# Performance work log

Measured on AMD Instinct MI355X. Metric: run time of the kernel, lower is better.

The kernel has to match this reference:

```python
import jax, jax.numpy as jnp
import numpy as np

N_NODES = 50000
N_EDGES = 800000
IN_DIM = 64
HEADS = 8
OUT_DIM = 8
CLAMP = 5.0
EPS = 1e-8


def _xavier(key, shape, fan_in, fan_out):
    std = float(np.sqrt(2.0 / (fan_in + fan_out)))
    return jax.random.normal(key, shape, jnp.float32) * std


def setup_inputs() -> dict:
    key = jax.random.key(0)
    ks = jax.random.split(key, 16)
    HD = HEADS * OUT_DIM
    return {
        "x": jax.random.normal(ks[0], (N_NODES, IN_DIM), jnp.float32),
        "edge_attr": jax.random.normal(ks[1], (N_EDGES, IN_DIM), jnp.float32),
        "edge_index": jax.random.randint(ks[2], (2, N_EDGES), 0, N_NODES, jnp.int64),
        "Wq": _xavier(ks[3], (IN_DIM, HD), IN_DIM, HD),
        "bq": jnp.zeros((HD,), jnp.float32),
        "Wk": _xavier(ks[4], (IN_DIM, HD), IN_DIM, HD),
        "bk": jnp.zeros((HD,), jnp.float32),
        "We": _xavier(ks[5], (IN_DIM, 2 * HD), IN_DIM, 2 * HD),
        "be": jnp.zeros((2 * HD,), jnp.float32),
        "Wv": _xavier(ks[6], (IN_DIM, HD), IN_DIM, HD),
        "bv": jnp.zeros((HD,), jnp.float32),
        "Aw": _xavier(ks[7], (OUT_DIM, HEADS, 1), OUT_DIM * HEADS, 1),
        "VeRow": _xavier(ks[8], (OUT_DIM, HEADS, OUT_DIM), OUT_DIM * HEADS, OUT_DIM),
    }


def _segment_softmax(score, seg, num_segments):
    # score: [E, H, 1], seg: [E] destination node ids
    m = jax.ops.segment_max(score, seg, num_segments=num_segments)
    m = jnp.where(jnp.isfinite(m), m, 0.0)  # empty segments -> -inf guard
    e = jnp.exp(score - m[seg])
    s = jax.ops.segment_sum(e, seg, num_segments=num_segments)
    return e / (s[seg] + 1e-16)


def reference(x, edge_attr, edge_index, Wq, bq, Wk, bk, We, be, Wv, bv, Aw, VeRow):
    n = x.shape[0]
    Q_h = (x @ Wq + bq).reshape(n, HEADS, OUT_DIM)
    K_h = (x @ Wk + bk).reshape(n, HEADS, OUT_DIM)
    V_h = (x @ Wv + bv).reshape(n, HEADS, OUT_DIM)
    E_proj = (edge_attr @ We + be).reshape(-1, HEADS, 2 * OUT_DIM)
    E_w, E_b = E_proj[:, :, :OUT_DIM], E_proj[:, :, OUT_DIM:]

    src, dst = edge_index[0], edge_index[1]
    score = K_h[src] + Q_h[dst]                       # [E, H, D]
    score = score * E_w
    # signed-sqrt
    score = jnp.sqrt(jax.nn.relu(score) + EPS) - jnp.sqrt(jax.nn.relu(-score) + EPS)
    score = score + E_b
    e_t = score                                       # act = Identity
    wE = score.reshape(score.shape[0], -1)            # [E, H*D]

    s = jnp.einsum('ehd,dhc->ehc', score, Aw)         # [E, H, 1]
    s = jnp.clip(s, -CLAMP, CLAMP)
    attn = _segment_softmax(s, dst, n)                # [E, H, 1]

    msg = V_h[src] * attn                             # [E, H, D]
    wV = jax.ops.segment_sum(msg, dst, num_segments=n)
    rowV = jax.ops.segment_sum(e_t * attn, dst, num_segments=n)
    wV = wV + jnp.einsum('nhd,dhc->nhc', rowV, VeRow)
    return wV, wE
```

## Files before the change

kernel.cpp:

```cpp
#include <hip/hip_runtime.h>
#include <math.h>

#define N_NODES 50000
#define N_EDGES 800000
#define CLAMP_V 5.0f
#define EPS_V   1e-8f

__global__ __launch_bounds__(192) void qkv_kernel(
    const float* __restrict__ x,
    const float* __restrict__ Wq, const float* __restrict__ bq,
    const float* __restrict__ Wk, const float* __restrict__ bk,
    const float* __restrict__ Wv, const float* __restrict__ bv,
    float* __restrict__ qkv)
{
  __shared__ float sW[64][192];
  __shared__ float sb[192];
  __shared__ float sa[16][68];
  const int t = threadIdx.x;
  for (int k = 0; k < 64; k++) {
    float w;
    if (t < 64)       w = Wq[k*64 + t];
    else if (t < 128) w = Wk[k*64 + (t-64)];
    else              w = Wv[k*64 + (t-128)];
    sW[k][t] = w;
  }
  sb[t] = (t < 64) ? bq[t] : (t < 128) ? bk[t-64] : bv[t-128];
  const int n0 = blockIdx.x * 16;
  for (int idx = t; idx < 256; idx += 192) {
    int node = idx >> 4, kq = idx & 15;
    *(float4*)&sa[node][kq*4] = *(const float4*)&x[(size_t)(n0+node)*64 + kq*4];
  }
  __syncthreads();
  float acc[16];
  #pragma unroll
  for (int j = 0; j < 16; j++) acc[j] = 0.f;
  for (int k4 = 0; k4 < 16; k4++) {
    float wq[4];
    #pragma unroll
    for (int q = 0; q < 4; q++) wq[q] = sW[k4*4+q][t];
    #pragma unroll
    for (int jh = 0; jh < 2; jh++) {
      float4 av[8];
      #pragma unroll
      for (int jj = 0; jj < 8; jj++) av[jj] = *(const float4*)&sa[jh*8+jj][k4*4];
      #pragma unroll
      for (int jj = 0; jj < 8; jj++) {
        acc[jh*8+jj] += av[jj].x*wq[0] + av[jj].y*wq[1] + av[jj].z*wq[2] + av[jj].w*wq[3];
      }
    }
  }
  const float b = sb[t];
  #pragma unroll
  for (int j = 0; j < 16; j++) qkv[(size_t)(n0+j)*192 + t] = acc[j] + b;
}

__global__ __launch_bounds__(256) void edge_kernel(
    const float* __restrict__ edge_attr,
    const int*   __restrict__ eidx,
    const float* __restrict__ We, const float* __restrict__ be,
    const float* __restrict__ Aw,
    const float* __restrict__ qkv,
    float* __restrict__ wE, float* __restrict__ sExp)
{
  __shared__ float sW[32][136];
  __shared__ float sA[128][32];
  __shared__ float sbe[128];
  __shared__ float sAw[64];
  const int t = threadIdx.x;
  const int e0 = blockIdx.x * 128;
  const int te = t >> 4;
  const int g = t & 15, h = g >> 1, dq = g & 1;
  const int cw = h*16 + dq*4, cb = cw + 8;
  const int cwp = cw + 8*(h>>2), cbp = cb + 8*(h>>2);
  const int swa = te & 3;
  float4 accw[8], accb[8];
  #pragma unroll
  for (int j = 0; j < 8; j++) { accw[j] = make_float4(0,0,0,0); accb[j] = make_float4(0,0,0,0); }
  if (t < 128)       sbe[t] = be[t];
  else if (t < 192)  sAw[t-128] = Aw[t-128];

  for (int ph = 0; ph < 2; ph++) {
    if (ph) __syncthreads();
    for (int i = t; i < 1024; i += 256) {
      int k = i >> 5, c = (i & 31) * 4;
      *(float4*)&sW[k][c + 8*(c>>6)] = *(const float4*)&We[(size_t)(ph*32+k)*128 + c];
    }
    for (int i = t; i < 1024; i += 256) {
      int e = i >> 3, kq = i & 7;
      *(float4*)&sA[e][(kq ^ ((e>>3)&3)) * 4] =
          *(const float4*)&edge_attr[(size_t)(e0+e)*64 + ph*32 + kq*4];
    }
    __syncthreads();
    for (int kq = 0; kq < 8; kq++) {
      float4 av[8];
      const int kcol = (kq ^ swa) * 4;
      #pragma unroll
      for (int j = 0; j < 8; j++) av[j] = *(const float4*)&sA[te*8+j][kcol];
      #pragma unroll
      for (int q = 0; q < 4; q++) {
        const int k = kq*4 + q;
        const float4 ww = *(const float4*)&sW[k][cwp];
        const float4 wb = *(const float4*)&sW[k][cbp];
        #pragma unroll
        for (int j = 0; j < 8; j++) {
          const float a = (q==0) ? av[j].x : (q==1) ? av[j].y : (q==2) ? av[j].z : av[j].w;
          accw[j].x += a*ww.x; accw[j].y += a*ww.y; accw[j].z += a*ww.z; accw[j].w += a*ww.w;
          accb[j].x += a*wb.x; accb[j].y += a*wb.y; accb[j].z += a*wb.z; accb[j].w += a*wb.w;
        }
      }
    }
  }

  const float4 bw = *(const float4*)&sbe[cw];
  const float4 bb = *(const float4*)&sbe[cb];
  const int d0 = dq * 4;
  const float awc0 = sAw[(d0+0)*8+h], awc1 = sAw[(d0+1)*8+h];
  const float awc2 = sAw[(d0+2)*8+h], awc3 = sAw[(d0+3)*8+h];
  #pragma unroll
  for (int j = 0; j < 8; j++) {
    const int e   = e0 + te*8 + j;
    const int src = eidx[e];
    const int dst = eidx[N_EDGES + e];
    const float4 kv = *(const float4*)&qkv[(size_t)src*192 + 64 + h*8 + d0];
    const float4 qv = *(const float4*)&qkv[(size_t)dst*192 +      h*8 + d0];
    const float s0 = (kv.x+qv.x)*(accw[j].x+bw.x);
    const float s1 = (kv.y+qv.y)*(accw[j].y+bw.y);
    const float s2 = (kv.z+qv.z)*(accw[j].z+bw.z);
    const float s3 = (kv.w+qv.w)*(accw[j].w+bw.w);
    const float r0 = sqrtf(fmaxf(s0,0.f)+EPS_V) - sqrtf(fmaxf(-s0,0.f)+EPS_V) + (accb[j].x+bb.x);
    const float r1 = sqrtf(fmaxf(s1,0.f)+EPS_V) - sqrtf(fmaxf(-s1,0.f)+EPS_V) + (accb[j].y+bb.y);
    const float r2 = sqrtf(fmaxf(s2,0.f)+EPS_V) - sqrtf(fmaxf(-s2,0.f)+EPS_V) + (accb[j].z+bb.z);
    const float r3 = sqrtf(fmaxf(s3,0.f)+EPS_V) - sqrtf(fmaxf(-s3,0.f)+EPS_V) + (accb[j].w+bb.w);
    *(float4*)&wE[(size_t)e*64 + h*8 + d0] = make_float4(r0,r1,r2,r3);
    float ps = r0*awc0 + r1*awc1 + r2*awc2 + r3*awc3;
    ps += __shfl_xor(ps, 1, 64);
    if (dq == 0) {
      const float sc = fminf(fmaxf(ps, -CLAMP_V), CLAMP_V);
      sExp[(size_t)e*8 + h] = expf(sc);
    }
  }
}

__global__ __launch_bounds__(256) void count_kernel(const int* __restrict__ eidx,
                                                    int* __restrict__ deg)
{
  const int e = blockIdx.x*256 + threadIdx.x;
  if (e < N_EDGES) atomicAdd(&deg[eidx[N_EDGES + e]], 1);
}

__global__ __launch_bounds__(1024) void scan_kernel(const int* __restrict__ deg,
                                                    int* __restrict__ row_start,
                                                    int* __restrict__ cursor)
{
  __shared__ int buf[1024];
  const int t = threadIdx.x;
  const int beg = t * 49;
  const int end = (beg + 49 < N_NODES) ? beg + 49 : N_NODES;
  int sum = 0;
  for (int i = beg; i < end; i++) sum += deg[i];
  buf[t] = sum;
  __syncthreads();
  for (int off = 1; off < 1024; off <<= 1) {
    const int v = (t >= off) ? buf[t-off] : 0;
    __syncthreads();
    buf[t] += v;
    __syncthreads();
  }
  int run = (t == 0) ? 0 : buf[t-1];
  for (int i = beg; i < end; i++) {
    const int d = deg[i];
    row_start[i] = run; cursor[i] = run; run += d;
  }
  if (t == 1023) row_start[N_NODES] = buf[1023];
}

__global__ __launch_bounds__(256) void scatter_kernel(const int* __restrict__ eidx,
                                                      int* __restrict__ cursor,
                                                      int* __restrict__ edge_ord,
                                                      int* __restrict__ src_perm)
{
  const int e = blockIdx.x*256 + threadIdx.x;
  if (e < N_EDGES) {
    const int pos = atomicAdd(&cursor[eidx[N_EDGES + e]], 1);
    edge_ord[pos] = e;
    src_perm[pos] = eidx[e];
  }
}

__global__ __launch_bounds__(256) void node_kernel(
    const int*   __restrict__ row_start,
    const int*   __restrict__ edge_ord,
    const int*   __restrict__ src_perm,
    const float* __restrict__ sExp,
    const float* __restrict__ qkv,
    const float* __restrict__ wE,
    const float* __restrict__ VeRow,
    float* __restrict__ wV)
{
  __shared__ float sVe[512];
  const int t = threadIdx.x;
  for (int i = t; i < 512; i += 256) sVe[i] = VeRow[i];
  __syncthreads();
  const int lane = t & 63;
  const int node = blockIdx.x*4 + (t >> 6);
  const int h = lane >> 3;
  const int rs = row_start[node], re = row_start[node+1];
  float accU = 0.f, accR = 0.f, accD = 0.f;
  int j = rs;
  for (; j + 4 <= re; j += 4) {
    const int e0 = edge_ord[j],   e1 = edge_ord[j+1];
    const int e2 = edge_ord[j+2], e3 = edge_ord[j+3];
    const int s0 = src_perm[j],   s1 = src_perm[j+1];
    const int s2 = src_perm[j+2], s3 = src_perm[j+3];
    const float w0 = sExp[(size_t)e0*8 + h], w1 = sExp[(size_t)e1*8 + h];
    const float w2 = sExp[(size_t)e2*8 + h], w3 = sExp[(size_t)e3*8 + h];
    const float t0 = __builtin_nontemporal_load(&wE[(size_t)e0*64 + lane]);
    const float t1 = __builtin_nontemporal_load(&wE[(size_t)e1*64 + lane]);
    const float t2 = __builtin_nontemporal_load(&wE[(size_t)e2*64 + lane]);
    const float t3 = __builtin_nontemporal_load(&wE[(size_t)e3*64 + lane]);
    const float v0 = qkv[(size_t)s0*192 + 128 + lane];
    const float v1 = qkv[(size_t)s1*192 + 128 + lane];
    const float v2 = qkv[(size_t)s2*192 + 128 + lane];
    const float v3 = qkv[(size_t)s3*192 + 128 + lane];
    accD += (w0 + w1) + (w2 + w3);
    accU += w0*v0; accU += w1*v1; accU += w2*v2; accU += w3*v3;
    accR += w0*t0; accR += w1*t1; accR += w2*t2; accR += w3*t3;
  }
  for (; j < re; j++) {
    const int eid = edge_ord[j];
    const int src = src_perm[j];
    const float w = sExp[(size_t)eid*8 + h];
    accD += w;
    accU += w * qkv[(size_t)src*192 + 128 + lane];
    accR += w * __builtin_nontemporal_load(&wE[(size_t)eid*64 + lane]);
  }
  float val = accU;
  #pragma unroll
  for (int dd = 0; dd < 8; dd++) {
    const float rv = __shfl(accR, h*8 + dd, 64);
    val += rv * sVe[dd*64 + lane];
  }
  wV[(size_t)node*64 + lane] = val * (1.0f / (accD + 1e-16f));
}

extern "C" void kernel_launch(void* const* d_in, const int* in_sizes, int n_in,
                              void* d_out, int out_size, void* d_ws, size_t ws_size,
                              hipStream_t stream)
{
  const float* x         = (const float*)d_in[0];
  const float* edge_attr = (const float*)d_in[1];
  const int*   eidx      = (const int*)  d_in[2];
  const float* Wq        = (const float*)d_in[3];
  const float* bq        = (const float*)d_in[4];
  const float* Wk        = (const float*)d_in[5];
  const float* bk        = (const float*)d_in[6];
  const float* We        = (const float*)d_in[7];
  const float* be        = (const float*)d_in[8];
  const float* Wv        = (const float*)d_in[9];
  const float* bv        = (const float*)d_in[10];
  const float* Aw        = (const float*)d_in[11];
  const float* VeRow     = (const float*)d_in[12];

  float* out = (float*)d_out;
  float* wV  = out;
  float* wE  = out + (size_t)N_NODES * 64;

  char* ws = (char*)d_ws;
  float* qkv      = (float*)(ws);
  float* sExp     = (float*)(ws + 38400000);
  int*   deg      = (int*)  (ws + 64000000);
  int*   row_start= (int*)  (ws + 64200000);
  int*   cursor   = (int*)  (ws + 64400208);
  int*   edge_ord = (int*)  (ws + 64600208);
  int*   src_perm = (int*)  (ws + 67800208);

  hipMemsetAsync(deg, 0, N_NODES * sizeof(int), stream);
  qkv_kernel    <<<3125,  192, 0, stream>>>(x, Wq, bq, Wk, bk, Wv, bv, qkv);
  edge_kernel   <<<6250,  256, 0, stream>>>(edge_attr, eidx, We, be, Aw, qkv, wE, sExp);
  count_kernel  <<<3125,  256, 0, stream>>>(eidx, deg);
  scan_kernel   <<<1,    1024, 0, stream>>>(deg, row_start, cursor);
  scatter_kernel<<<3125,  256, 0, stream>>>(eidx, cursor, edge_ord, src_perm);
  node_kernel   <<<12500, 256, 0, stream>>>(row_start, edge_ord, src_perm, sExp, qkv, wE, VeRow, wV);
}
```

Baseline: 866.8 us.

## Split node aggregation across two waves per node, vectorize weight loads

The node kernel now assigns two wavefronts to each node, each handling alternating edges, and combines partial sums through shared memory before the final projection. This doubles the in-flight gathers per node to hide memory latency, at the cost of a block-wide barrier and twice the number of blocks. The qkv kernel loads weights into shared memory as float4, the edge kernel gets a minimum-occupancy launch bound, and sExp reads become nontemporal loads.

Result: slower. 909.2 us (+4.9%).

```diff
diff --git a/kernel.cpp b/kernel.cpp
--- a/kernel.cpp
+++ b/kernel.cpp
@@ -17,12 +17,12 @@
   __shared__ float sb[192];
   __shared__ float sa[16][68];
   const int t = threadIdx.x;
-  for (int k = 0; k < 64; k++) {
-    float w;
-    if (t < 64)       w = Wq[k*64 + t];
-    else if (t < 128) w = Wk[k*64 + (t-64)];
-    else              w = Wv[k*64 + (t-128)];
-    sW[k][t] = w;
+  for (int i = t; i < 3072; i += 192) {
+    const int w = i >> 10;
+    const int r = (i >> 4) & 63;
+    const int c4 = (i & 15) * 4;
+    const float* W = (w == 0) ? Wq : (w == 1) ? Wk : Wv;
+    *(float4*)&sW[r][w*64 + c4] = *(const float4*)&W[r*64 + c4];
   }
   sb[t] = (t < 64) ? bq[t] : (t < 128) ? bk[t-64] : bv[t-128];
   const int n0 = blockIdx.x * 16;
@@ -54,7 +54,7 @@
   for (int j = 0; j < 16; j++) qkv[(size_t)(n0+j)*192 + t] = acc[j] + b;
 }
 
-__global__ __launch_bounds__(256) void edge_kernel(
+__global__ __launch_bounds__(256, 4) void edge_kernel(
     const float* __restrict__ edge_attr,
     const int*   __restrict__ eidx,
     const float* __restrict__ We, const float* __restrict__ be,
@@ -198,22 +198,27 @@
     float* __restrict__ wV)
 {
   __shared__ float sVe[512];
+  __shared__ float red[2][64][3];
   const int t = threadIdx.x;
   for (int i = t; i < 512; i += 256) sVe[i] = VeRow[i];
-  __syncthreads();
   const int lane = t & 63;
-  const int node = blockIdx.x*4 + (t >> 6);
+  const int w    = t >> 6;
+  const int nl   = w >> 1;
+  const int par  = w & 1;
+  const int node = blockIdx.x*2 + nl;
   const int h = lane >> 3;
   const int rs = row_start[node], re = row_start[node+1];
   float accU = 0.f, accR = 0.f, accD = 0.f;
-  int j = rs;
-  for (; j + 4 <= re; j += 4) {
-    const int e0 = edge_ord[j],   e1 = edge_ord[j+1];
-    const int e2 = edge_ord[j+2], e3 = edge_ord[j+3];
-    const int s0 = src_perm[j],   s1 = src_perm[j+1];
-    const int s2 = src_perm[j+2], s3 = src_perm[j+3];
-    const float w0 = sExp[(size_t)e0*8 + h], w1 = sExp[(size_t)e1*8 + h];
-    const float w2 = sExp[(size_t)e2*8 + h], w3 = sExp[(size_t)e3*8 + h];
+  int j = rs + par;
+  for (; j + 6 < re; j += 8) {
+    const int e0 = edge_ord[j],   e1 = edge_ord[j+2];
+    const int e2 = edge_ord[j+4], e3 = edge_ord[j+6];
+    const int s0 = src_perm[j],   s1 = src_perm[j+2];
+    const int s2 = src_perm[j+4], s3 = src_perm[j+6];
+    const float w0 = __builtin_nontemporal_load(&sExp[(size_t)e0*8 + h]);
+    const float w1 = __builtin_nontemporal_load(&sExp[(size_t)e1*8 + h]);
+    const float w2 = __builtin_nontemporal_load(&sExp[(size_t)e2*8 + h]);
+    const float w3 = __builtin_nontemporal_load(&sExp[(size_t)e3*8 + h]);
     const float t0 = __builtin_nontemporal_load(&wE[(size_t)e0*64 + lane]);
     const float t1 = __builtin_nontemporal_load(&wE[(size_t)e1*64 + lane]);
     const float t2 = __builtin_nontemporal_load(&wE[(size_t)e2*64 + lane]);
@@ -226,21 +231,30 @@
     accU += w0*v0; accU += w1*v1; accU += w2*v2; accU += w3*v3;
     accR += w0*t0; accR += w1*t1; accR += w2*t2; accR += w3*t3;
   }
-  for (; j < re; j++) {
+  for (; j < re; j += 2) {
     const int eid = edge_ord[j];
     const int src = src_perm[j];
-    const float w = sExp[(size_t)eid*8 + h];
-    accD += w;
-    accU += w * qkv[(size_t)src*192 + 128 + lane];
-    accR += w * __builtin_nontemporal_load(&wE[(size_t)eid*64 + lane]);
-  }
-  float val = accU;
-  #pragma unroll
-  for (int dd = 0; dd < 8; dd++) {
-    const float rv = __shfl(accR, h*8 + dd, 64);
-    val += rv * sVe[dd*64 + lane];
-  }
-  wV[(size_t)node*64 + lane] = val * (1.0f / (accD + 1e-16f));
+    const float ww = __builtin_nontemporal_load(&sExp[(size_t)eid*8 + h]);
+    accD += ww;
+    accU += ww * qkv[(size_t)src*192 + 128 + lane];
+    accR += ww * __builtin_nontemporal_load(&wE[(size_t)eid*64 + lane]);
+  }
+  if (par == 1) {
+    red[nl][lane][0] = accU; red[nl][lane][1] = accR; red[nl][lane][2] = accD;
+  }
+  __syncthreads();
+  if (par == 0) {
+    accU += red[nl][lane][0];
+    accR += red[nl][lane][1];
+    accD += red[nl][lane][2];
+    float val = accU;
+    #pragma unroll
+    for (int dd = 0; dd < 8; dd++) {
+      const float rv = __shfl(accR, h*8 + dd, 64);
+      val += rv * sVe[dd*64 + lane];
+    }
+    wV[(size_t)node*64 + lane] = val * (1.0f / (accD + 1e-16f));
+  }
 }
 
 extern "C" void kernel_launch(void* const* d_in, const int* in_sizes, int n_in,
@@ -280,5 +294,5 @@
   count_kernel  <<<3125,  256, 0, stream>>>(eidx, deg);
   scan_kernel   <<<1,    1024, 0, stream>>>(deg, row_start, cursor);
   scatter_kernel<<<3125,  256, 0, stream>>>(eidx, cursor, edge_ord, src_perm);
-  node_kernel   <<<12500, 256, 0, stream>>>(row_start, edge_ord, src_perm, sExp, qkv, wE, VeRow, wV);
-}
+  node_kernel   <<<25000, 256, 0, stream>>>(row_start, edge_ord, src_perm, sExp, qkv, wE, VeRow, wV);
+}
```
